# Performance work log

Hardware: AMD Instinct MI355X
Metric: run time of the kernel (lower is better)

Reference implementation:

```python
import jax, jax.numpy as jnp
import numpy as np

B, S, D, FD = 2, 2048, 1024, 4096
EPS_LN = 1e-5


def _l2norm(x):
    n = jnp.linalg.norm(x, axis=-1, keepdims=True)
    return x / jnp.maximum(n, 1e-12)


def _layernorm(x, w, b):
    m = x.mean(-1, keepdims=True)
    v = ((x - m) ** 2).mean(-1, keepdims=True)
    return (x - m) / jnp.sqrt(v + EPS_LN) * w + b


def _spl(x, mu_w, mu_b, gate, proto):
    # cosine-similarity gated linear (SparseProtoLinear)
    scores = _l2norm(x) @ _l2norm(proto).T          # [..., out]
    rw = jax.nn.relu(scores - gate)
    comp = x @ mu_w.T + mu_b
    return comp * rw


def _rotate_half(x):
    h = x.shape[-1] // 2
    return jnp.concatenate([-x[..., h:], x[..., :h]], axis=-1)


def _forward(x, cos, sin,
             ln1_w, ln1_b, ln2_w, ln2_b,
             qkv_mu, qkv_proto, qkv_bias, qkv_gate,
             o_mu, o_proto, o_bias, o_gate,
             f1_mu, f1_proto, f1_bias, f1_gate,
             f2_mu, f2_proto, f2_bias, f2_gate,
             pt_qkv, pt_o, pt_f1, pt_f2,
             pln_qkv_w, pln_qkv_b, pln_o_w, pln_o_b,
             pln_f1_w, pln_f1_b, pln_f2_w, pln_f2_b,
             prev_qkv, prev_o, prev_f1, prev_f2):
    # effective protos: proto_weight + LN(Linear(prev_proto))
    eff_qkv = qkv_proto + _layernorm(prev_qkv @ pt_qkv.T, pln_qkv_w, pln_qkv_b)
    eff_o   = o_proto   + _layernorm(prev_o   @ pt_o.T,   pln_o_w,   pln_o_b)
    eff_f1  = f1_proto  + _layernorm(prev_f1  @ pt_f1.T,  pln_f1_w,  pln_f1_b)
    eff_f2  = f2_proto  + _layernorm(prev_f2  @ pt_f2.T,  pln_f2_w,  pln_f2_b)

    # attention
    attn_in = _layernorm(x, ln1_w, ln1_b)
    m_qkv = _spl(attn_in, qkv_mu, qkv_bias, qkv_gate, eff_qkv)   # [B,S,3D]
    q, k, v = jnp.split(m_qkv, 3, axis=-1)
    c = cos[None]; s = sin[None]
    q = q * c + _rotate_half(q) * s
    k = k * c + _rotate_half(k) * s
    scale = 1.0 / jnp.sqrt(jnp.asarray(D, x.dtype))
    scores = jnp.einsum('bqd,bkd->bqk', q, k) * scale            # [B,S,S]
    causal = jnp.tril(jnp.ones((S, S), dtype=bool))
    scores = jnp.where(causal[None], scores, jnp.finfo(x.dtype).min)
    attn = jax.nn.softmax(scores, axis=-1)
    attn_out = jnp.einsum('bqk,bkd->bqd', attn, v)
    m_o = _spl(attn_out, o_mu, o_bias, o_gate, eff_o)
    x1 = x + m_o

    # ffn (DynamicInfiniteExpert)
    ffn_in = _layernorm(x1, ln2_w, ln2_b)
    m1 = _spl(ffn_in, f1_mu, f1_bias, f1_gate, eff_f1)           # [B,S,FD]
    h = jax.nn.relu(m1)
    m2 = _spl(h, f2_mu, f2_bias, f2_gate, eff_f2)                # [B,S,D]
    return x1 + m2


def setup_inputs() -> dict:
    key = jax.random.key(0)
    ks = iter(jax.random.split(key, 64))

    def nrm(shape, scale=1.0):
        return jax.random.normal(next(ks), shape, dtype=jnp.float32) * scale

    # RoPE tables
    pos = np.arange(S, dtype=np.float32)
    inv_freq = 1.0 / (10000.0 ** (np.arange(0, D, 2, dtype=np.float32) / D))
    freqs = np.outer(pos, inv_freq)
    emb = np.concatenate([freqs, freqs], axis=-1)
    cos = jnp.asarray(np.cos(emb)); sin = jnp.asarray(np.sin(emb))

    sD = 1.0 / np.sqrt(D); sF = 1.0 / np.sqrt(FD)
    inp = {
        'x': nrm((B, S, D)), 'cos': cos, 'sin': sin,
        'ln1_w': jnp.ones((D,)), 'ln1_b': jnp.zeros((D,)),
        'ln2_w': jnp.ones((D,)), 'ln2_b': jnp.zeros((D,)),
        'qkv_mu': nrm((3 * D, D), sD), 'qkv_proto': nrm((3 * D, D), sD),
        'qkv_bias': jnp.zeros((3 * D,)), 'qkv_gate': jnp.zeros((3 * D,)),
        'o_mu': nrm((D, D), sD), 'o_proto': nrm((D, D), sD),
        'o_bias': jnp.zeros((D,)), 'o_gate': jnp.zeros((D,)),
        'f1_mu': nrm((FD, D), sD), 'f1_proto': nrm((FD, D), sD),
        'f1_bias': jnp.zeros((FD,)), 'f1_gate': jnp.zeros((FD,)),
        'f2_mu': nrm((D, FD), sF), 'f2_proto': nrm((D, FD), sF),
        'f2_bias': jnp.zeros((D,)), 'f2_gate': jnp.zeros((D,)),
        'pt_qkv': nrm((D, D), sD), 'pt_o': nrm((D, D), sD),
        'pt_f1': nrm((D, D), sD), 'pt_f2': nrm((FD, FD), sF),
        'pln_qkv_w': jnp.ones((D,)), 'pln_qkv_b': jnp.zeros((D,)),
        'pln_o_w': jnp.ones((D,)), 'pln_o_b': jnp.zeros((D,)),
        'pln_f1_w': jnp.ones((D,)), 'pln_f1_b': jnp.zeros((D,)),
        'pln_f2_w': jnp.ones((FD,)), 'pln_f2_b': jnp.zeros((FD,)),
        'prev_qkv': nrm((3 * D, D), sD), 'prev_o': nrm((D, D), sD),
        'prev_f1': nrm((FD, D), sD), 'prev_f2': nrm((D, FD), sF),
    }
    return inp


def reference(x, cos, sin,
              ln1_w, ln1_b, ln2_w, ln2_b,
              qkv_mu, qkv_proto, qkv_bias, qkv_gate,
              o_mu, o_proto, o_bias, o_gate,
              f1_mu, f1_proto, f1_bias, f1_gate,
              f2_mu, f2_proto, f2_bias, f2_gate,
              pt_qkv, pt_o, pt_f1, pt_f2,
              pln_qkv_w, pln_qkv_b, pln_o_w, pln_o_b,
              pln_f1_w, pln_f1_b, pln_f2_w, pln_f2_b,
              prev_qkv, prev_o, prev_f1, prev_f2):
    return _forward(x, cos, sin, ln1_w, ln1_b, ln2_w, ln2_b,
                    qkv_mu, qkv_proto, qkv_bias, qkv_gate,
                    o_mu, o_proto, o_bias, o_gate,
                    f1_mu, f1_proto, f1_bias, f1_gate,
                    f2_mu, f2_proto, f2_bias, f2_gate,
                    pt_qkv, pt_o, pt_f1, pt_f2,
                    pln_qkv_w, pln_qkv_b, pln_o_w, pln_o_b,
                    pln_f1_w, pln_f1_b, pln_f2_w, pln_f2_b,
                    prev_qkv, prev_o, prev_f1, prev_f2)
```

## Files before the change

kernel.cpp:

```cpp
#include <hip/hip_runtime.h>
#include <cstdint>

typedef unsigned short u16;
typedef __attribute__((ext_vector_type(8))) short sh8;
typedef __attribute__((ext_vector_type(4))) float f32x4;

struct __align__(8) us4 { u16 x, y, z, w; };

__device__ __forceinline__ u16 f2bf(float f) {
  unsigned u = __float_as_uint(f);
  u += 0x7FFFu + ((u >> 16) & 1u);
  return (u16)(u >> 16);
}
__device__ __forceinline__ float bf2f(u16 h) {
  return __uint_as_float((unsigned)h << 16);
}

__device__ __forceinline__ float blk_sum(float v, float* red) {
#pragma unroll
  for (int o = 32; o; o >>= 1) v += __shfl_xor(v, o);
  __syncthreads();
  if ((threadIdx.x & 63) == 0) red[threadIdx.x >> 6] = v;
  __syncthreads();
  return red[0] + red[1] + red[2] + red[3];
}
__device__ __forceinline__ float blk_max(float v, float* red) {
#pragma unroll
  for (int o = 32; o; o >>= 1) v = fmaxf(v, __shfl_xor(v, o));
  __syncthreads();
  if ((threadIdx.x & 63) == 0) red[threadIdx.x >> 6] = v;
  __syncthreads();
  return fmaxf(fmaxf(red[0], red[1]), fmaxf(red[2], red[3]));
}

__global__ void cvt_bf16(const float* __restrict__ S, u16* __restrict__ D, long n4) {
  long i = (long)blockIdx.x * blockDim.x + threadIdx.x;
  if (i >= n4) return;
  float4 v = ((const float4*)S)[i];
  us4 o; o.x = f2bf(v.x); o.y = f2bf(v.y); o.z = f2bf(v.z); o.w = f2bf(v.w);
  ((us4*)D)[i] = o;
}

__global__ void cvt_str(const float* __restrict__ S, u16* __restrict__ Dst,
                        int K, long ostride) {
  int row = blockIdx.x;
  const float* s = S + (size_t)row * K;
  u16* d = Dst + (size_t)row * ostride;
  for (int c = threadIdx.x << 2; c < K; c += 1024) {
    float4 v = *(const float4*)(s + c);
    us4 o; o.x = f2bf(v.x); o.y = f2bf(v.y); o.z = f2bf(v.z); o.w = f2bf(v.w);
    *(us4*)(d + c) = o;
  }
}

__global__ void fillv(float* __restrict__ o, long n, float v) {
  long i = (long)blockIdx.x * blockDim.x + threadIdx.x;
  if (i < n) o[i] = v;
}

#define GL16(gp, lp)                                                        \
  __builtin_amdgcn_global_load_lds(                                         \
      (const __attribute__((address_space(1))) void*)(gp),                  \
      (__attribute__((address_space(3))) void*)(lp), 16, 0, 0)

#define G256_PROLOG()                                                          \
  extern __shared__ u16 lds[];                                                 \
  int tid = threadIdx.x;                                                       \
  int wid = tid >> 6, lane = tid & 63;                                         \
  int wm = wid >> 2, wn = wid & 3;                                             \
  int bm = blockIdx.x, bn = blockIdx.y;                                        \
  int k0s = 0, nt;                                                             \
  if (kchunk) {                                                                \
    k0s = blockIdx.z * kchunk;                                                 \
    nt = kchunk >> 5;                                                          \
  } else {                                                                     \
    nt = K >> 5;                                                               \
  }                                                                            \
  const size_t baseArow = (size_t)bm * 256;                                    \
  const size_t baseBrow = (size_t)bn * 256;                                    \
  int ci = (wid << 6) + lane;                                                  \
  int rowS = ci >> 2;                                                          \
  int kcS = (ci ^ (ci >> 3)) & 3;                                              \
  const u16* gA0 = A + (baseArow + rowS) * lda + k0s + kcS * 8;                \
  const u16* gA1 = gA0 + (size_t)128 * lda;                                    \
  const u16* gB0 = B + (baseBrow + rowS) * ldb + k0s + kcS * 8;                \
  const u16* gB1 = gB0 + (size_t)128 * ldb;                                    \
  u16* dBase = lds + (wid << 9);                                               \
  int l15 = lane & 15, l4 = lane >> 4;                                         \
  int aoff[8], boff[4];                                                        \
  _Pragma("unroll") for (int fr = 0; fr < 8; ++fr) {                           \
    int by = (wm * 128 + fr * 16 + l15) * 64 + l4 * 16;                        \
    aoff[fr] = (by ^ (((by >> 7) & 3) << 4)) >> 1;                             \
  }                                                                            \
  _Pragma("unroll") for (int fc = 0; fc < 4; ++fc) {                           \
    int by = (wn * 64 + fc * 16 + l15) * 64 + l4 * 16;                         \
    boff[fc] = 8192 + ((by ^ (((by >> 7) & 3) << 4)) >> 1);                    \
  }                                                                            \
  f32x4 acc[8][4];                                                             \
  const f32x4 zf = {0.f, 0.f, 0.f, 0.f};                                       \
  _Pragma("unroll") for (int i = 0; i < 8; ++i)                                \
    _Pragma("unroll") for (int j = 0; j < 4; ++j) acc[i][j] = zf;

#define STAGE256(ts)                                                  \
  do {                                                                \
    int ss_ = (ts) & 3;                                               \
    int kk_ = (ts) << 5;                                              \
    u16* d_ = dBase + ss_ * 16384;                                    \
    GL16(gA0 + kk_, d_);                                              \
    GL16(gA1 + kk_, d_ + 4096);                                       \
    GL16(gB0 + kk_, d_ + 8192);                                       \
    GL16(gB1 + kk_, d_ + 12288);                                      \
  } while (0)

#define G256_KLOOP()                                                           \
  STAGE256(0);                                                                 \
  STAGE256(1);                                                                 \
  STAGE256(2);                                                                 \
  asm volatile("s_waitcnt vmcnt(8)" ::: "memory");                             \
  __builtin_amdgcn_s_barrier();                                                \
  __builtin_amdgcn_sched_barrier(0);                                           \
  for (int t = 0; t < nt; ++t) {                                               \
    int ts = t + 3;                                                            \
    if (ts < nt) STAGE256(ts);                                                 \
    const u16* sl = lds + (t & 3) * 16384;                                     \
    sh8 af[8], bfv[4];                                                         \
    _Pragma("unroll") for (int fc = 0; fc < 4; ++fc)                           \
        bfv[fc] = *(const sh8*)(sl + boff[fc]);                                \
    _Pragma("unroll") for (int fr = 0; fr < 8; ++fr)                           \
        af[fr] = *(const sh8*)(sl + aoff[fr]);                                 \
    __builtin_amdgcn_s_setprio(1);                                             \
    _Pragma("unroll") for (int fr = 0; fr < 8; ++fr)                           \
      _Pragma("unroll") for (int fc = 0; fc < 4; ++fc)                         \
        acc[fr][fc] = __builtin_amdgcn_mfma_f32_16x16x32_bf16(                 \
            af[fr], bfv[fc], acc[fr][fc], 0, 0, 0);                            \
    __builtin_amdgcn_s_setprio(0);                                             \
    int rem = nt - 2 - t;                                                      \
    if (rem >= 2)      asm volatile("s_waitcnt vmcnt(8)" ::: "memory");        \
    else if (rem == 1) asm volatile("s_waitcnt vmcnt(4)" ::: "memory");        \
    else if (rem == 0) asm volatile("s_waitcnt vmcnt(0)" ::: "memory");        \
    if (t < nt - 1) {                                                          \
      __builtin_amdgcn_s_barrier();                                            \
      __builtin_amdgcn_sched_barrier(0);                                       \
    }                                                                          \
  }

template <typename CT>
__global__ __launch_bounds__(512, 1) void gemm256(
    const u16* __restrict__ A, const u16* __restrict__ B, CT* __restrict__ C,
    int M, int N, int K, int lda, int ldb, int kchunk) {
  if (kchunk) C += (size_t)blockIdx.z * M * (size_t)N;
  G256_PROLOG();
  G256_KLOOP();
  int cr = l4 << 2, cc = l15;
  const size_t rbase = baseArow + wm * 128 + cr;
  const size_t cbase = baseBrow + wn * 64 + cc;
#pragma unroll
  for (int fr = 0; fr < 8; ++fr)
#pragma unroll
    for (int fc = 0; fc < 4; ++fc) {
      size_t cb = (rbase + fr * 16) * (size_t)N + cbase + fc * 16;
#pragma unroll
      for (int r = 0; r < 4; ++r) {
        float v = acc[fr][fc][r];
        if constexpr (sizeof(CT) == 2) C[cb + (size_t)r * N] = (CT)f2bf(v);
        else                           C[cb + (size_t)r * N] = v;
      }
    }
}

__global__ __launch_bounds__(512, 1) void gemm256_spl(
    const u16* __restrict__ A, const u16* __restrict__ B, u16* __restrict__ out,
    int M, int N, int K, int lda, int ldb, int kchunk,
    const float* __restrict__ bias, const float* __restrict__ gate,
    const float* __restrict__ rn, const float* __restrict__ cn, int relu_out) {
  G256_PROLOG();
  G256_KLOOP();
  int cr = l4 << 2, cc = l15;
  const size_t rbase = baseArow + wm * 128 + cr;
  const size_t cbase = baseBrow + wn * 64 + cc;
  const int F = N >> 1;
  bool evenL = (cc & 1) == 0;
  float bb[4], gg[4], nn[4];
  int ft[4];
#pragma unroll
  for (int fc = 0; fc < 4; ++fc) {
    ft[fc] = (int)((cbase + fc * 16) >> 1);
    bb[fc] = bias[ft[fc]]; gg[fc] = gate[ft[fc]]; nn[fc] = cn[ft[fc]];
  }
#pragma unroll
  for (int fr = 0; fr < 8; ++fr)
#pragma unroll
    for (int r = 0; r < 4; ++r) {
      size_t row = rbase + fr * 16 + r;
      float rr = rn[row];
#pragma unroll
      for (int fc = 0; fc < 4; ++fc) {
        float mine = acc[fr][fc][r];
        float other = __shfl_xor(mine, 1);
        float comp = evenL ? mine : other;
        float dots = evenL ? other : mine;
        float sc = dots / (rr * nn[fc]);
        float v = (comp + bb[fc]) * fmaxf(sc - gg[fc], 0.f);
        if (relu_out) v = fmaxf(v, 0.f);
        if (evenL) out[row * (size_t)F + ft[fc]] = f2bf(v);
      }
    }
}

template <typename CT>
__global__ __launch_bounds__(256, 2) void gemm_bt(
    const u16* __restrict__ A, const u16* __restrict__ B, CT* __restrict__ C,
    int M, int N, int K, int lda, int ldb,
    int mode, long zsA, long zsB, long zsC) {
  int bm, bn;
  int z = blockIdx.z;
  if (mode == 3) {
    int t = blockIdx.x;
    int m = (int)floorf((sqrtf(8.f * t + 1.f) - 1.f) * 0.5f);
    while ((m + 1) * (m + 2) / 2 <= t) ++m;
    while (m * (m + 1) / 2 > t) --m;
    bm = m; bn = t - m * (m + 1) / 2;
  } else {
    bm = blockIdx.x; bn = blockIdx.y;
  }
  int k0s = 0, k0e = K;
  if (mode == 1) {
    int kc = K / gridDim.z;
    k0s = z * kc; k0e = k0s + kc;
    C += (size_t)z * M * (size_t)N;
  } else if (mode == 2 || mode == 3) {
    A += (size_t)z * zsA; B += (size_t)z * zsB; C += (size_t)z * zsC;
  } else if (mode == 4) {
    A += (size_t)z * zsA; B += (size_t)z * zsB; C += (size_t)z * zsC;
    k0e = (bm + 1) * 128;
  } else if (mode == 5) {
    int Mz = (int)((zsB >> (z * 16)) & 0xFFFF);
    if (bm * 128 >= Mz) return;
    A += (size_t)z * zsA; B += (size_t)z * 1048576; C += (size_t)z * zsC;
  }

  __shared__ __align__(16) u16 As[128 * 32];
  __shared__ __align__(16) u16 Bs[128 * 32];
  int tid = threadIdx.x, wid = tid >> 6, lane = tid & 63;
  int wr = (wid >> 1) << 6, wc = (wid & 1) << 6;
  int lr = lane & 15, lk = (lane >> 4) << 3;

  f32x4 acc[4][4];
  const f32x4 zf = {0.f, 0.f, 0.f, 0.f};
#pragma unroll
  for (int i = 0; i < 4; ++i)
#pragma unroll
    for (int j = 0; j < 4; ++j) acc[i][j] = zf;

  int r0 = tid >> 2, c0 = (tid & 3) << 3;
  const size_t baseA = (size_t)bm * 128, baseB = (size_t)bn * 128;
  const u16* Ab = A + baseA * lda;
  const u16* Bp = B + baseB * ldb;

  for (int k0 = k0s; k0 < k0e; k0 += 32) {
    GL16(Ab + (size_t)r0 * lda + k0 + c0, As + (wid << 9));
    GL16(Ab + (size_t)(64 + r0) * lda + k0 + c0, As + 2048 + (wid << 9));
    GL16(Bp + (size_t)r0 * ldb + k0 + c0, Bs + (wid << 9));
    GL16(Bp + (size_t)(64 + r0) * ldb + k0 + c0, Bs + 2048 + (wid << 9));
    __syncthreads();
    sh8 af[4], bfr[4];
#pragma unroll
    for (int f = 0; f < 4; ++f) {
      af[f]  = *(const sh8*)(As + (wr + f * 16 + lr) * 32 + lk);
      bfr[f] = *(const sh8*)(Bs + (wc + f * 16 + lr) * 32 + lk);
    }
#pragma unroll
    for (int i = 0; i < 4; ++i)
#pragma unroll
      for (int j = 0; j < 4; ++j)
        acc[i][j] = __builtin_amdgcn_mfma_f32_16x16x32_bf16(af[i], bfr[j], acc[i][j], 0, 0, 0);
    __syncthreads();
  }

  int cr = (lane >> 4) << 2, cc = lane & 15;
#pragma unroll
  for (int i = 0; i < 4; ++i)
#pragma unroll
    for (int j = 0; j < 4; ++j) {
      size_t cb = (baseA + wr + i * 16 + cr) * (size_t)N + (baseB + wc + j * 16 + cc);
#pragma unroll
      for (int r = 0; r < 4; ++r) {
        float v = acc[i][j][r];
        if constexpr (sizeof(CT) == 2) C[cb + (size_t)r * N] = (CT)f2bf(v);
        else                           C[cb + (size_t)r * N] = v;
      }
    }
}

__global__ void ln_rows(const float* __restrict__ X, const float* __restrict__ w,
                        const float* __restrict__ b, u16* __restrict__ Y,
                        float* __restrict__ norms, int C) {
  __shared__ float red[4];
  int row = blockIdx.x;
  const float* x = X + (size_t)row * C;
  int nv = C >> 2;
  float s = 0.f, ss = 0.f;
  for (int i = threadIdx.x; i < nv; i += 256) {
    float4 v = ((const float4*)x)[i];
    s += v.x + v.y + v.z + v.w;
    ss += v.x * v.x + v.y * v.y + v.z * v.z + v.w * v.w;
  }
  s = blk_sum(s, red);
  ss = blk_sum(ss, red);
  float mean = s / C;
  float inv = rsqrtf(fmaxf(ss / C - mean * mean, 0.f) + 1e-5f);
  float nrm = 0.f;
  for (int i = threadIdx.x; i < nv; i += 256) {
    float4 v = ((const float4*)x)[i];
    float4 wv = ((const float4*)w)[i];
    float4 bv = ((const float4*)b)[i];
    float y0 = (v.x - mean) * inv * wv.x + bv.x;
    float y1 = (v.y - mean) * inv * wv.y + bv.y;
    float y2 = (v.z - mean) * inv * wv.z + bv.z;
    float y3 = (v.w - mean) * inv * wv.w + bv.w;
    nrm += y0 * y0 + y1 * y1 + y2 * y2 + y3 * y3;
    us4 o; o.x = f2bf(y0); o.y = f2bf(y1); o.z = f2bf(y2); o.w = f2bf(y3);
    ((us4*)(Y + (size_t)row * C))[i] = o;
  }
  nrm = blk_sum(nrm, red);
  if (threadIdx.x == 0) norms[row] = fmaxf(sqrtf(nrm), 1e-12f);
}

__global__ void ln_add_norm(const u16* __restrict__ T0, const u16* __restrict__ T1,
                            const float* __restrict__ P,
                            const float* __restrict__ w, const float* __restrict__ b,
                            u16* __restrict__ E, float* __restrict__ norms, int C,
                            long ostride) {
  __shared__ float red[4];
  int row = blockIdx.x;
  const us4* t0 = (const us4*)(T0 + (size_t)row * C);
  const us4* t1 = T1 ? (const us4*)(T1 + (size_t)row * C) : nullptr;
  const float* p = P + (size_t)row * C;
  int nv = C >> 2;
  float s = 0.f, ss = 0.f;
  for (int i = threadIdx.x; i < nv; i += 256) {
    us4 v = t0[i];
    float f0 = bf2f(v.x), f1 = bf2f(v.y), f2 = bf2f(v.z), f3 = bf2f(v.w);
    if (t1) {
      us4 v1 = t1[i];
      f0 += bf2f(v1.x); f1 += bf2f(v1.y); f2 += bf2f(v1.z); f3 += bf2f(v1.w);
    }
    s += f0 + f1 + f2 + f3;
    ss += f0 * f0 + f1 * f1 + f2 * f2 + f3 * f3;
  }
  s = blk_sum(s, red);
  ss = blk_sum(ss, red);
  float mean = s / C;
  float inv = rsqrtf(fmaxf(ss / C - mean * mean, 0.f) + 1e-5f);
  float nrm = 0.f;
  for (int i = threadIdx.x; i < nv; i += 256) {
    us4 v = t0[i];
    float f0 = bf2f(v.x), f1 = bf2f(v.y), f2 = bf2f(v.z), f3 = bf2f(v.w);
    if (t1) {
      us4 v1 = t1[i];
      f0 += bf2f(v1.x); f1 += bf2f(v1.y); f2 += bf2f(v1.z); f3 += bf2f(v1.w);
    }
    float4 pv = ((const float4*)p)[i];
    float4 wv = ((const float4*)w)[i];
    float4 bv = ((const float4*)b)[i];
    float y0 = pv.x + (f0 - mean) * inv * wv.x + bv.x;
    float y1 = pv.y + (f1 - mean) * inv * wv.y + bv.y;
    float y2 = pv.z + (f2 - mean) * inv * wv.z + bv.z;
    float y3 = pv.w + (f3 - mean) * inv * wv.w + bv.w;
    nrm += y0 * y0 + y1 * y1 + y2 * y2 + y3 * y3;
    us4 o; o.x = f2bf(y0); o.y = f2bf(y1); o.z = f2bf(y2); o.w = f2bf(y3);
    *(us4*)(E + (size_t)row * ostride + (i << 2)) = o;
  }
  nrm = blk_sum(nrm, red);
  if (threadIdx.x == 0) norms[row] = fmaxf(sqrtf(nrm), 1e-12f);
}

__global__ void rownorm_bf(const u16* __restrict__ X, float* __restrict__ norms, int C) {
  __shared__ float red[4];
  int row = blockIdx.x;
  const us4* x = (const us4*)(X + (size_t)row * C);
  int nv = C >> 2;
  float nrm = 0.f;
  for (int i = threadIdx.x; i < nv; i += 256) {
    us4 v = x[i];
    float a = bf2f(v.x), b = bf2f(v.y), c = bf2f(v.z), d = bf2f(v.w);
    nrm += a * a + b * b + c * c + d * d;
  }
  nrm = blk_sum(nrm, red);
  if (threadIdx.x == 0) norms[row] = fmaxf(sqrtf(nrm), 1e-12f);
}

__device__ __forceinline__ void epi4(const u16* gr, int C, int c, float rr,
                                     const float* bias, const float* gate,
                                     const float* cn, float* o) {
  us4 cv = *(const us4*)(gr + c);
  us4 dv = *(const us4*)(gr + C + c);
  float4 bv = *(const float4*)(bias + c);
  float4 gv = *(const float4*)(gate + c);
  float4 nv = *(const float4*)(cn + c);
  float cf[4] = {bf2f(cv.x), bf2f(cv.y), bf2f(cv.z), bf2f(cv.w)};
  float df[4] = {bf2f(dv.x), bf2f(dv.y), bf2f(dv.z), bf2f(dv.w)};
  float bb[4] = {bv.x, bv.y, bv.z, bv.w};
  float gg[4] = {gv.x, gv.y, gv.z, gv.w};
  float nn[4] = {nv.x, nv.y, nv.z, nv.w};
#pragma unroll
  for (int j = 0; j < 4; ++j) {
    float sc = df[j] / (rr * nn[j]);
    o[j] = (cf[j] + bb[j]) * fmaxf(sc - gg[j], 0.f);
  }
}

__global__ void rope_ip(u16* __restrict__ MQ, const float* __restrict__ CT_,
                        const float* __restrict__ ST_) {
  long t = (long)blockIdx.x * blockDim.x + threadIdx.x;
  int i = (int)(t & 511);
  long row = t >> 9;
  int s = (int)(row & 2047);
  u16* base = MQ + row * 3072;
  float c0 = CT_[(size_t)s * 1024 + i], c1 = CT_[(size_t)s * 1024 + 512 + i];
  float s0 = ST_[(size_t)s * 1024 + i], s1 = ST_[(size_t)s * 1024 + 512 + i];
  float q0 = bf2f(base[i]), q1 = bf2f(base[512 + i]);
  base[i]        = f2bf(q0 * c0 - q1 * s0);
  base[512 + i]  = f2bf(q1 * c1 + q0 * s1);
  float k0 = bf2f(base[1024 + i]), k1 = bf2f(base[1536 + i]);
  base[1024 + i] = f2bf(k0 * c0 - k1 * s0);
  base[1536 + i] = f2bf(k1 * c1 + k0 * s1);
}

__global__ void spl_o_ln_row(const u16* __restrict__ G, const float* __restrict__ bias,
                             const float* __restrict__ gate, const float* __restrict__ rn,
                             const float* __restrict__ cn, const float* __restrict__ xres,
                             const float* __restrict__ lw, const float* __restrict__ lb,
                             float* __restrict__ X1, u16* __restrict__ Y,
                             float* __restrict__ rn_ffn) {
  __shared__ float red[4];
  int r = blockIdx.x;
  int c = threadIdx.x << 2;
  const u16* gr = G + (size_t)r * 2048;
  float o[4];
  epi4(gr, 1024, c, rn[r], bias, gate, cn, o);
  float4 rv = *(const float4*)(xres + (size_t)r * 1024 + c);
  o[0] += rv.x; o[1] += rv.y; o[2] += rv.z; o[3] += rv.w;
  float4 xo = {o[0], o[1], o[2], o[3]};
  *(float4*)(X1 + (size_t)r * 1024 + c) = xo;
  float s = o[0] + o[1] + o[2] + o[3];
  float ss = o[0] * o[0] + o[1] * o[1] + o[2] * o[2] + o[3] * o[3];
  s = blk_sum(s, red);
  ss = blk_sum(ss, red);
  float mean = s * (1.f / 1024.f);
  float inv = rsqrtf(fmaxf(ss * (1.f / 1024.f) - mean * mean, 0.f) + 1e-5f);
  float4 wv = *(const float4*)(lw + c);
  float4 bv = *(const float4*)(lb + c);
  float ww[4] = {wv.x, wv.y, wv.z, wv.w}, bb[4] = {bv.x, bv.y, bv.z, bv.w};
  float nrm = 0.f;
  us4 ov;
  u16* op = (u16*)&ov;
#pragma unroll
  for (int j = 0; j < 4; ++j) {
    float y = (o[j] - mean) * inv * ww[j] + bb[j];
    nrm += y * y;
    op[j] = f2bf(y);
  }
  *(us4*)(Y + (size_t)r * 1024 + c) = ov;
  nrm = blk_sum(nrm, red);
  if (threadIdx.x == 0) rn_ffn[r] = fmaxf(sqrtf(nrm), 1e-12f);
}

__global__ void spl_epi_p(const u16* __restrict__ G0, const u16* __restrict__ G1,
                          const float* __restrict__ bias, const float* __restrict__ gate,
                          const float* __restrict__ rn, const float* __restrict__ cn,
                          const float* __restrict__ resid, float* __restrict__ out) {
  int r = blockIdx.x;
  int c = threadIdx.x << 2;
  size_t rowb = (size_t)r * 2048;
  us4 c0 = *(const us4*)(G0 + rowb + c);
  us4 c1 = *(const us4*)(G1 + rowb + c);
  us4 d0 = *(const us4*)(G0 + rowb + 1024 + c);
  us4 d1 = *(const us4*)(G1 + rowb + 1024 + c);
  float4 bv = *(const float4*)(bias + c);
  float4 gv = *(const float4*)(gate + c);
  float4 nv = *(const float4*)(cn + c);
  float4 rv = *(const float4*)(resid + (size_t)r * 1024 + c);
  float rr = rn[r];
  float cf[4] = {bf2f(c0.x) + bf2f(c1.x), bf2f(c0.y) + bf2f(c1.y),
                 bf2f(c0.z) + bf2f(c1.z), bf2f(c0.w) + bf2f(c1.w)};
  float df[4] = {bf2f(d0.x) + bf2f(d1.x), bf2f(d0.y) + bf2f(d1.y),
                 bf2f(d0.z) + bf2f(d1.z), bf2f(d0.w) + bf2f(d1.w)};
  float bb[4] = {bv.x, bv.y, bv.z, bv.w};
  float gg[4] = {gv.x, gv.y, gv.z, gv.w};
  float nn[4] = {nv.x, nv.y, nv.z, nv.w};
  float re[4] = {rv.x, rv.y, rv.z, rv.w};
  float4 ov;
  float* op = (float*)&ov;
#pragma unroll
  for (int j = 0; j < 4; ++j) {
    float sc = df[j] / (rr * nn[j]);
    op[j] = (cf[j] + bb[j]) * fmaxf(sc - gg[j], 0.f) + re[j];
  }
  *(float4*)(out + (size_t)r * 1024 + c) = ov;
}

__global__ void vtrans(const u16* __restrict__ MQ, u16* __restrict__ VT) {
  __shared__ u16 tile[32][33];
  int b = blockIdx.z;
  int s0 = blockIdx.x << 5, d0 = blockIdx.y << 5;
  int tx = threadIdx.x, ty = threadIdx.y;
  for (int r = ty; r < 32; r += 8)
    tile[r][tx] = MQ[((size_t)(b * 2048 + s0 + r)) * 3072 + 2048 + d0 + tx];
  __syncthreads();
  for (int r = ty; r < 32; r += 8)
    VT[(size_t)b * 1024 * 2048 + (size_t)(d0 + r) * 2048 + s0 + tx] = tile[tx][r];
}

__global__ void softmax_causal(const float* __restrict__ S, u16* __restrict__ P) {
  __shared__ float red[4];
  int b = blockIdx.x >> 11;
  int q = blockIdx.x & 2047;
  const float* row = S + ((size_t)b << 22) + (size_t)q * 2048;
  u16* prow = P + ((size_t)b << 22) + (size_t)q * 2048;
  int nv = q + 1;
  int wcap = ((q >> 7) + 1) << 7;
  int base = threadIdx.x * 8;
  float e[8];
  float m = -3.4e38f;
  float xv[8];
  bool live = base < nv;
  if (live) {
    float4 a = *(const float4*)(row + base);
    float4 bq = *(const float4*)(row + base + 4);
    xv[0] = a.x; xv[1] = a.y; xv[2] = a.z; xv[3] = a.w;
    xv[4] = bq.x; xv[5] = bq.y; xv[6] = bq.z; xv[7] = bq.w;
#pragma unroll
    for (int j = 0; j < 8; ++j) {
      xv[j] *= 0.03125f;
      if (base + j < nv) m = fmaxf(m, xv[j]);
    }
  }
  m = blk_max(m, red);
  float ssum = 0.f;
#pragma unroll
  for (int j = 0; j < 8; ++j) {
    e[j] = (live && base + j < nv) ? __expf(xv[j] - m) : 0.f;
    ssum += e[j];
  }
  ssum = blk_sum(ssum, red);
  float invs = 1.f / ssum;
  if (base < wcap) {
    us4 o;
    o.x = f2bf(e[0] * invs); o.y = f2bf(e[1] * invs);
    o.z = f2bf(e[2] * invs); o.w = f2bf(e[3] * invs);
    ((us4*)prow)[threadIdx.x * 2] = o;
    o.x = f2bf(e[4] * invs); o.y = f2bf(e[5] * invs);
    o.z = f2bf(e[6] * invs); o.w = f2bf(e[7] * invs);
    ((us4*)prow)[threadIdx.x * 2 + 1] = o;
  }
}

extern "C" void kernel_launch(void* const* d_in, const int* in_sizes, int n_in,
                              void* d_out, int out_size, void* d_ws, size_t ws_size,
                              hipStream_t stream) {
  (void)in_sizes;
  const float* x         = (const float*)d_in[0];
  const float* cosT      = (const float*)d_in[1];
  const float* sinT      = (const float*)d_in[2];
  const float* ln1_w     = (const float*)d_in[3];
  const float* ln1_b     = (const float*)d_in[4];
  const float* ln2_w     = (const float*)d_in[5];
  const float* ln2_b     = (const float*)d_in[6];
  const float* qkv_mu    = (const float*)d_in[7];
  const float* qkv_proto = (const float*)d_in[8];
  const float* qkv_bias  = (const float*)d_in[9];
  const float* qkv_gate  = (const float*)d_in[10];
  const float* o_mu      = (const float*)d_in[11];
  const float* o_proto   = (const float*)d_in[12];
  const float* o_bias    = (const float*)d_in[13];
  const float* o_gate    = (const float*)d_in[14];
  const float* f1_mu     = (const float*)d_in[15];
  const float* f1_proto  = (const float*)d_in[16];
  const float* f1_bias   = (const float*)d_in[17];
  const float* f1_gate   = (const float*)d_in[18];
  const float* f2_mu     = (const float*)d_in[19];
  const float* f2_proto  = (const float*)d_in[20];
  const float* f2_bias   = (const float*)d_in[21];
  const float* f2_gate   = (const float*)d_in[22];
  const float* pt_qkv    = (const float*)d_in[23];
  const float* pt_o      = (const float*)d_in[24];
  const float* pt_f1     = (const float*)d_in[25];
  const float* pt_f2     = (const float*)d_in[26];
  const float* pln_qkv_w = (const float*)d_in[27];
  const float* pln_qkv_b = (const float*)d_in[28];
  const float* pln_o_w   = (const float*)d_in[29];
  const float* pln_o_b   = (const float*)d_in[30];
  const float* pln_f1_w  = (const float*)d_in[31];
  const float* pln_f1_b  = (const float*)d_in[32];
  const float* pln_f2_w  = (const float*)d_in[33];
  const float* pln_f2_b  = (const float*)d_in[34];
  const float* prev_qkv  = (const float*)d_in[35];
  const float* prev_o    = (const float*)d_in[36];
  const float* prev_f1   = (const float*)d_in[37];
  const float* prev_f2   = (const float*)d_in[38];

  const long D = 1024, TD = 3072, FD = 4096, R = 4096;

  char* W = (char*)d_ws;
  size_t off = 0;
  auto alloc = [&](size_t bytes) {
    void* p = W + off;
    off = (off + bytes + 255) & ~(size_t)255;
    return p;
  };
  char* GOUT = (char*)alloc(67108864);
  u16*  RC   = (u16*)alloc(33554432);
  u16*  wq   = (u16*)alloc(2 * TD * D * 2);
  u16*  wo   = (u16*)alloc(2 * D * D * 2);
  u16*  wf1  = (u16*)alloc(2 * FD * D * 2);
  u16*  wf2  = (u16*)alloc(2 * D * FD * 2);
  float* X1  = (float*)alloc(R * D * 4);
  u16*  P1   = (u16*)alloc(R * D * 2);
  u16*  VT   = (u16*)alloc(2 * D * 2048 * 2);
  u16*  AOB  = (u16*)alloc(R * D * 2);
  float* pnq     = (float*)alloc(TD * 4);
  float* pno     = (float*)alloc(D * 4);
  float* pnf1    = (float*)alloc(FD * 4);
  float* pnf2    = (float*)alloc(D * 4);
  float* rn_ain  = (float*)alloc(R * 4);
  float* rn_aout = (float*)alloc(R * 4);
  float* rn_ffn  = (float*)alloc(R * 4);
  float* rn_h    = (float*)alloc(R * 4);
  size_t need = off;

  if (n_in < 39 || need > ws_size) {
    long n = out_size;
    fillv<<<dim3((unsigned)((n + 255) / 256)), 256, 0, stream>>>((float*)d_out, n, 12345.0f);
    return;
  }

  u16* SA = (u16*)GOUT;
  u16* SB = (u16*)(GOUT + 25165824);
  float* SCORES = (float*)GOUT;
  u16* PB = (u16*)(GOUT + 33554432);

  auto cvt = [&](const float* s, u16* d, long n) {
    long n4 = n >> 2;
    cvt_bf16<<<dim3((unsigned)((n4 + 255) / 256)), 256, 0, stream>>>(s, d, n4);
  };

  cvt(prev_f1,  SA,            FD * D);
  cvt(prev_qkv, SA + 4194304,  TD * D);
  cvt(prev_o,   SA + 8388608,  D * D);
  cvt(pt_f1,    SB,            D * D);
  cvt(pt_qkv,   SB + 1048576,  D * D);
  cvt(pt_o,     SB + 2097152,  D * D);
  {
    long Mz = 4096L | (3072L << 16) | (1024L << 32);
    gemm_bt<u16><<<dim3(32, 8, 3), 256, 0, stream>>>(
        SA, SB, RC, 4096, 1024, 1024, 1024, 1024, 5, 4194304, Mz, 4194304);
  }
  ln_add_norm<<<4096, 256, 0, stream>>>(RC, nullptr, f1_proto, pln_f1_w, pln_f1_b,
                                        wf1 + 1024, pnf1, 1024, 2048);
  ln_add_norm<<<3072, 256, 0, stream>>>(RC + 4194304, nullptr, qkv_proto, pln_qkv_w,
                                        pln_qkv_b, wq + 1024, pnq, 1024, 2048);
  ln_add_norm<<<1024, 256, 0, stream>>>(RC + 8388608, nullptr, o_proto, pln_o_w,
                                        pln_o_b, wo + (size_t)D * D, pno, 1024, 1024);
  cvt(prev_f2, SA, D * FD);
  cvt(pt_f2,   SB, (long)FD * FD);
  gemm_bt<u16><<<dim3(8, 32, 2), 256, 0, stream>>>(
      SA, SB, RC, 1024, 4096, 4096, 4096, 4096, 1, 0, 0, 0);
  ln_add_norm<<<1024, 256, 0, stream>>>(RC, RC + 4194304, f2_proto, pln_f2_w, pln_f2_b,
                                        wf2 + (size_t)D * FD, pnf2, 4096, 4096);
  cvt_str<<<3072, 256, 0, stream>>>(qkv_mu, wq, 1024, 2048);
  cvt_str<<<4096, 256, 0, stream>>>(f1_mu, wf1, 1024, 2048);
  cvt(o_mu,   wo, D * D);
  cvt(f2_mu,  wf2, D * FD);

  ln_rows<<<4096, 256, 0, stream>>>(x, ln1_w, ln1_b, P1, rn_ain, 1024);
  gemm256_spl<<<dim3(16, 24), 512, 131072, stream>>>(
      P1, wq, RC, 4096, 6144, 1024, 1024, 1024, 0,
      qkv_bias, qkv_gate, rn_ain, pnq, 0);
  rope_ip<<<dim3((unsigned)((R * 512) / 256)), 256, 0, stream>>>(RC, cosT, sinT);

  vtrans<<<dim3(64, 32, 2), dim3(32, 8), 0, stream>>>(RC, VT);
  gemm_bt<float><<<dim3(136, 1, 2), 256, 0, stream>>>(
      RC, RC + 1024, SCORES, 2048, 2048, 1024, 3072, 3072,
      3, 2048L * 3072, 2048L * 3072, 1L << 22);
  softmax_causal<<<4096, 256, 0, stream>>>(SCORES, PB);
  gemm_bt<u16><<<dim3(16, 8, 2), 256, 0, stream>>>(
      PB, VT, AOB, 2048, 1024, 2048, 2048, 2048,
      4, 1L << 22, 1024L * 2048, 2048L * 1024);
  rownorm_bf<<<4096, 256, 0, stream>>>(AOB, rn_aout, 1024);

  gemm_bt<u16><<<dim3(32, 16, 1), 256, 0, stream>>>(
      AOB, wo, (u16*)GOUT, 4096, 2048, 1024, 1024, 1024, 0, 0, 0, 0);
  spl_o_ln_row<<<4096, 256, 0, stream>>>(
      (u16*)GOUT, o_bias, o_gate, rn_aout, pno, x, ln2_w, ln2_b, X1, P1, rn_ffn);

  gemm256_spl<<<dim3(16, 32), 512, 131072, stream>>>(
      P1, wf1, RC, 4096, 8192, 1024, 1024, 1024, 0,
      f1_bias, f1_gate, rn_ffn, pnf1, 1);
  rownorm_bf<<<4096, 256, 0, stream>>>(RC, rn_h, 4096);
  gemm256<u16><<<dim3(16, 8, 2), 512, 131072, stream>>>(
      RC, wf2, (u16*)GOUT, 4096, 2048, 4096, 4096, 4096, 2048);
  spl_epi_p<<<4096, 256, 0, stream>>>(
      (u16*)GOUT, (u16*)GOUT + 8388608, f2_bias, f2_gate, rn_h, pnf2,
      X1, (float*)d_out);
}
```

Baseline: 636.4 us.

## Split SPL epilogues out of GEMMs, batch conversions, store inverse norms

```diff
diff --git a/kernel.cpp b/kernel.cpp
--- a/kernel.cpp
+++ b/kernel.cpp
@@ -14,6 +14,9 @@
 }
 __device__ __forceinline__ float bf2f(u16 h) {
   return __uint_as_float((unsigned)h << 16);
+}
+__device__ __forceinline__ float invnorm(float nrm) {
+  return fminf(rsqrtf(nrm), 1e12f);
 }
 
 __device__ __forceinline__ float blk_sum(float v, float* red) {
@@ -33,29 +36,23 @@
   return fmaxf(fmaxf(red[0], red[1]), fmaxf(red[2], red[3]));
 }
 
-__global__ void cvt_bf16(const float* __restrict__ S, u16* __restrict__ D, long n4) {
-  long i = (long)blockIdx.x * blockDim.x + threadIdx.x;
-  if (i >= n4) return;
-  float4 v = ((const float4*)S)[i];
-  us4 o; o.x = f2bf(v.x); o.y = f2bf(v.y); o.z = f2bf(v.z); o.w = f2bf(v.w);
-  ((us4*)D)[i] = o;
-}
-
-__global__ void cvt_str(const float* __restrict__ S, u16* __restrict__ Dst,
-                        int K, long ostride) {
-  int row = blockIdx.x;
-  const float* s = S + (size_t)row * K;
-  u16* d = Dst + (size_t)row * ostride;
-  for (int c = threadIdx.x << 2; c < K; c += 1024) {
-    float4 v = *(const float4*)(s + c);
-    us4 o; o.x = f2bf(v.x); o.y = f2bf(v.y); o.z = f2bf(v.z); o.w = f2bf(v.w);
-    *(us4*)(d + c) = o;
-  }
-}
-
 __global__ void fillv(float* __restrict__ o, long n, float v) {
   long i = (long)blockIdx.x * blockDim.x + threadIdx.x;
   if (i < n) o[i] = v;
+}
+
+struct CvtN10 {
+  const float* s[10];
+  u16* d[10];
+  long n4[10];
+};
+__global__ void cvt_many(CvtN10 c) {
+  int z = blockIdx.y;
+  long i = (long)blockIdx.x * blockDim.x + threadIdx.x;
+  if (i >= c.n4[z]) return;
+  float4 v = ((const float4*)c.s[z])[i];
+  us4 o; o.x = f2bf(v.x); o.y = f2bf(v.y); o.z = f2bf(v.z); o.w = f2bf(v.w);
+  ((us4*)c.d[z])[i] = o;
 }
 
 #define GL16(gp, lp)                                                        \
@@ -168,45 +165,6 @@
     }
 }
 
-__global__ __launch_bounds__(512, 1) void gemm256_spl(
-    const u16* __restrict__ A, const u16* __restrict__ B, u16* __restrict__ out,
-    int M, int N, int K, int lda, int ldb, int kchunk,
-    const float* __restrict__ bias, const float* __restrict__ gate,
-    const float* __restrict__ rn, const float* __restrict__ cn, int relu_out) {
-  G256_PROLOG();
-  G256_KLOOP();
-  int cr = l4 << 2, cc = l15;
-  const size_t rbase = baseArow + wm * 128 + cr;
-  const size_t cbase = baseBrow + wn * 64 + cc;
-  const int F = N >> 1;
-  bool evenL = (cc & 1) == 0;
-  float bb[4], gg[4], nn[4];
-  int ft[4];
-#pragma unroll
-  for (int fc = 0; fc < 4; ++fc) {
-    ft[fc] = (int)((cbase + fc * 16) >> 1);
-    bb[fc] = bias[ft[fc]]; gg[fc] = gate[ft[fc]]; nn[fc] = cn[ft[fc]];
-  }
-#pragma unroll
-  for (int fr = 0; fr < 8; ++fr)
-#pragma unroll
-    for (int r = 0; r < 4; ++r) {
-      size_t row = rbase + fr * 16 + r;
-      float rr = rn[row];
-#pragma unroll
-      for (int fc = 0; fc < 4; ++fc) {
-        float mine = acc[fr][fc][r];
-        float other = __shfl_xor(mine, 1);
-        float comp = evenL ? mine : other;
-        float dots = evenL ? other : mine;
-        float sc = dots / (rr * nn[fc]);
-        float v = (comp + bb[fc]) * fmaxf(sc - gg[fc], 0.f);
-        if (relu_out) v = fmaxf(v, 0.f);
-        if (evenL) out[row * (size_t)F + ft[fc]] = f2bf(v);
-      }
-    }
-}
-
 template <typename CT>
 __global__ __launch_bounds__(256, 2) void gemm_bt(
     const u16* __restrict__ A, const u16* __restrict__ B, CT* __restrict__ C,
@@ -323,14 +281,13 @@
     ((us4*)(Y + (size_t)row * C))[i] = o;
   }
   nrm = blk_sum(nrm, red);
-  if (threadIdx.x == 0) norms[row] = fmaxf(sqrtf(nrm), 1e-12f);
+  if (threadIdx.x == 0) norms[row] = invnorm(nrm);
 }
 
 __global__ void ln_add_norm(const u16* __restrict__ T0, const u16* __restrict__ T1,
                             const float* __restrict__ P,
                             const float* __restrict__ w, const float* __restrict__ b,
-                            u16* __restrict__ E, float* __restrict__ norms, int C,
-                            long ostride) {
+                            u16* __restrict__ E, float* __restrict__ norms, int C) {
   __shared__ float red[4];
   int row = blockIdx.x;
   const us4* t0 = (const us4*)(T0 + (size_t)row * C);
@@ -369,10 +326,40 @@
     float y3 = pv.w + (f3 - mean) * inv * wv.w + bv.w;
     nrm += y0 * y0 + y1 * y1 + y2 * y2 + y3 * y3;
     us4 o; o.x = f2bf(y0); o.y = f2bf(y1); o.z = f2bf(y2); o.w = f2bf(y3);
-    *(us4*)(E + (size_t)row * ostride + (i << 2)) = o;
+    *(us4*)(E + (size_t)row * C + (i << 2)) = o;
   }
   nrm = blk_sum(nrm, red);
-  if (threadIdx.x == 0) norms[row] = fmaxf(sqrtf(nrm), 1e-12f);
+  if (threadIdx.x == 0) norms[row] = invnorm(nrm);
+}
+
+struct Lan3 {
+  const u16* T[3];
+  const float* P[3]; const float* w[3]; const float* b[3];
+  u16* E[3]; float* nr[3]; int M[3];
+};
+__global__ void lan_many(Lan3 L) {
+  __shared__ float red[4];
+  int z = blockIdx.y;
+  int row = blockIdx.x;
+  if (row >= L.M[z]) return;
+  int i = threadIdx.x;
+  us4 v = ((const us4*)(L.T[z] + (size_t)row * 1024))[i];
+  float f0 = bf2f(v.x), f1 = bf2f(v.y), f2 = bf2f(v.z), f3 = bf2f(v.w);
+  float s = blk_sum(f0 + f1 + f2 + f3, red);
+  float ss = blk_sum(f0 * f0 + f1 * f1 + f2 * f2 + f3 * f3, red);
+  float mean = s * (1.f / 1024.f);
+  float inv = rsqrtf(fmaxf(ss * (1.f / 1024.f) - mean * mean, 0.f) + 1e-5f);
+  float4 pv = ((const float4*)(L.P[z] + (size_t)row * 1024))[i];
+  float4 wv = ((const float4*)L.w[z])[i];
+  float4 bv = ((const float4*)L.b[z])[i];
+  float y0 = pv.x + (f0 - mean) * inv * wv.x + bv.x;
+  float y1 = pv.y + (f1 - mean) * inv * wv.y + bv.y;
+  float y2 = pv.z + (f2 - mean) * inv * wv.z + bv.z;
+  float y3 = pv.w + (f3 - mean) * inv * wv.w + bv.w;
+  us4 o; o.x = f2bf(y0); o.y = f2bf(y1); o.z = f2bf(y2); o.w = f2bf(y3);
+  ((us4*)(L.E[z] + (size_t)row * 1024))[i] = o;
+  float nrm = blk_sum(y0 * y0 + y1 * y1 + y2 * y2 + y3 * y3, red);
+  if (threadIdx.x == 0) L.nr[z][row] = invnorm(nrm);
 }
 
 __global__ void rownorm_bf(const u16* __restrict__ X, float* __restrict__ norms, int C) {
@@ -387,7 +374,7 @@
     nrm += a * a + b * b + c * c + d * d;
   }
   nrm = blk_sum(nrm, red);
-  if (threadIdx.x == 0) norms[row] = fmaxf(sqrtf(nrm), 1e-12f);
+  if (threadIdx.x == 0) norms[row] = invnorm(nrm);
 }
 
 __device__ __forceinline__ void epi4(const u16* gr, int C, int c, float rr,
@@ -405,26 +392,78 @@
   float nn[4] = {nv.x, nv.y, nv.z, nv.w};
 #pragma unroll
   for (int j = 0; j < 4; ++j) {
-    float sc = df[j] / (rr * nn[j]);
+    float sc = df[j] * (rr * nn[j]);
     o[j] = (cf[j] + bb[j]) * fmaxf(sc - gg[j], 0.f);
   }
 }
 
-__global__ void rope_ip(u16* __restrict__ MQ, const float* __restrict__ CT_,
-                        const float* __restrict__ ST_) {
-  long t = (long)blockIdx.x * blockDim.x + threadIdx.x;
-  int i = (int)(t & 511);
-  long row = t >> 9;
-  int s = (int)(row & 2047);
-  u16* base = MQ + row * 3072;
-  float c0 = CT_[(size_t)s * 1024 + i], c1 = CT_[(size_t)s * 1024 + 512 + i];
-  float s0 = ST_[(size_t)s * 1024 + i], s1 = ST_[(size_t)s * 1024 + 512 + i];
-  float q0 = bf2f(base[i]), q1 = bf2f(base[512 + i]);
-  base[i]        = f2bf(q0 * c0 - q1 * s0);
-  base[512 + i]  = f2bf(q1 * c1 + q0 * s1);
-  float k0 = bf2f(base[1024 + i]), k1 = bf2f(base[1536 + i]);
-  base[1024 + i] = f2bf(k0 * c0 - k1 * s0);
-  base[1536 + i] = f2bf(k1 * c1 + k0 * s1);
+__global__ void spl_rope_row(const u16* __restrict__ G, const float* __restrict__ bias,
+                             const float* __restrict__ gate, const float* __restrict__ rn,
+                             const float* __restrict__ cn, const float* __restrict__ CT_,
+                             const float* __restrict__ ST_, u16* __restrict__ MQ) {
+  int r = blockIdx.x;
+  int s = r & 2047;
+  const u16* gr = G + (size_t)r * 6144;
+  u16* outr = MQ + (size_t)r * 3072;
+  float rr = rn[r];
+  int t = threadIdx.x;
+
+  int qk = (t >> 7);
+  int c = qk * 1024 + ((t & 127) << 2);
+  int d = c - qk * 1024;
+  float a0[4], a1[4];
+  epi4(gr, 3072, c, rr, bias, gate, cn, a0);
+  epi4(gr, 3072, c + 512, rr, bias, gate, cn, a1);
+  const float* ct = CT_ + (size_t)s * 1024;
+  const float* st = ST_ + (size_t)s * 1024;
+  float4 c0 = *(const float4*)(ct + d);
+  float4 s0 = *(const float4*)(st + d);
+  float4 c1 = *(const float4*)(ct + d + 512);
+  float4 s1 = *(const float4*)(st + d + 512);
+  float cc0[4] = {c0.x, c0.y, c0.z, c0.w}, ss0[4] = {s0.x, s0.y, s0.z, s0.w};
+  float cc1[4] = {c1.x, c1.y, c1.z, c1.w}, ss1[4] = {s1.x, s1.y, s1.z, s1.w};
+  us4 o0, o1;
+  o0.x = f2bf(a0[0] * cc0[0] - a1[0] * ss0[0]);
+  o0.y = f2bf(a0[1] * cc0[1] - a1[1] * ss0[1]);
+  o0.z = f2bf(a0[2] * cc0[2] - a1[2] * ss0[2]);
+  o0.w = f2bf(a0[3] * cc0[3] - a1[3] * ss0[3]);
+  o1.x = f2bf(a1[0] * cc1[0] + a0[0] * ss1[0]);
+  o1.y = f2bf(a1[1] * cc1[1] + a0[1] * ss1[1]);
+  o1.z = f2bf(a1[2] * cc1[2] + a0[2] * ss1[2]);
+  o1.w = f2bf(a1[3] * cc1[3] + a0[3] * ss1[3]);
+  *(us4*)(outr + c) = o0;
+  *(us4*)(outr + c + 512) = o1;
+
+  int cv_ = 2048 + (t << 2);
+  float vv[4];
+  epi4(gr, 3072, cv_, rr, bias, gate, cn, vv);
+  us4 ov; ov.x = f2bf(vv[0]); ov.y = f2bf(vv[1]); ov.z = f2bf(vv[2]); ov.w = f2bf(vv[3]);
+  *(us4*)(outr + cv_) = ov;
+}
+
+__global__ void spl_f1_row(const u16* __restrict__ G, const float* __restrict__ bias,
+                           const float* __restrict__ gate, const float* __restrict__ rn,
+                           const float* __restrict__ cn, u16* __restrict__ H,
+                           float* __restrict__ rn_h) {
+  __shared__ float red[4];
+  int r = blockIdx.x;
+  const u16* gr = G + (size_t)r * 8192;
+  u16* hr = H + (size_t)r * 4096;
+  float rr = rn[r];
+  float nrm = 0.f;
+  for (int c = threadIdx.x << 2; c < 4096; c += 1024) {
+    float o[4];
+    epi4(gr, 4096, c, rr, bias, gate, cn, o);
+#pragma unroll
+    for (int j = 0; j < 4; ++j) {
+      o[j] = fmaxf(o[j], 0.f);
+      nrm += o[j] * o[j];
+    }
+    us4 ov; ov.x = f2bf(o[0]); ov.y = f2bf(o[1]); ov.z = f2bf(o[2]); ov.w = f2bf(o[3]);
+    *(us4*)(hr + c) = ov;
+  }
+  nrm = blk_sum(nrm, red);
+  if (threadIdx.x == 0) rn_h[r] = invnorm(nrm);
 }
 
 __global__ void spl_o_ln_row(const u16* __restrict__ G, const float* __restrict__ bias,
@@ -463,7 +502,7 @@
   }
   *(us4*)(Y + (size_t)r * 1024 + c) = ov;
   nrm = blk_sum(nrm, red);
-  if (threadIdx.x == 0) rn_ffn[r] = fmaxf(sqrtf(nrm), 1e-12f);
+  if (threadIdx.x == 0) rn_ffn[r] = invnorm(nrm);
 }
 
 __global__ void spl_epi_p(const u16* __restrict__ G0, const u16* __restrict__ G1,
@@ -494,7 +533,7 @@
   float* op = (float*)&ov;
 #pragma unroll
   for (int j = 0; j < 4; ++j) {
-    float sc = df[j] / (rr * nn[j]);
+    float sc = df[j] * (rr * nn[j]);
     op[j] = (cf[j] + bb[j]) * fmaxf(sc - gg[j], 0.f) + re[j];
   }
   *(float4*)(out + (size_t)r * 1024 + c) = ov;
@@ -640,44 +679,51 @@
   float* SCORES = (float*)GOUT;
   u16* PB = (u16*)(GOUT + 33554432);
 
-  auto cvt = [&](const float* s, u16* d, long n) {
-    long n4 = n >> 2;
-    cvt_bf16<<<dim3((unsigned)((n4 + 255) / 256)), 256, 0, stream>>>(s, d, n4);
-  };
-
-  cvt(prev_f1,  SA,            FD * D);
-  cvt(prev_qkv, SA + 4194304,  TD * D);
-  cvt(prev_o,   SA + 8388608,  D * D);
-  cvt(pt_f1,    SB,            D * D);
-  cvt(pt_qkv,   SB + 1048576,  D * D);
-  cvt(pt_o,     SB + 2097152,  D * D);
+  {
+    CvtN10 c;
+    c.s[0] = prev_f1;  c.d[0] = SA;            c.n4[0] = (FD * D) >> 2;
+    c.s[1] = prev_qkv; c.d[1] = SA + 4194304;  c.n4[1] = (TD * D) >> 2;
+    c.s[2] = prev_o;   c.d[2] = SA + 8388608;  c.n4[2] = (D * D) >> 2;
+    c.s[3] = pt_f1;    c.d[3] = SB;            c.n4[3] = (D * D) >> 2;
+    c.s[4] = pt_qkv;   c.d[4] = SB + 1048576;  c.n4[4] = (D * D) >> 2;
+    c.s[5] = pt_o;     c.d[5] = SB + 2097152;  c.n4[5] = (D * D) >> 2;
+    c.s[6] = qkv_mu;   c.d[6] = wq;            c.n4[6] = (TD * D) >> 2;
+    c.s[7] = f1_mu;    c.d[7] = wf1;           c.n4[7] = (FD * D) >> 2;
+    c.s[8] = o_mu;     c.d[8] = wo;            c.n4[8] = (D * D) >> 2;
+    c.s[9] = f2_mu;    c.d[9] = wf2;           c.n4[9] = (D * FD) >> 2;
+    cvt_many<<<dim3(4096, 10), 256, 0, stream>>>(c);
+  }
   {
     long Mz = 4096L | (3072L << 16) | (1024L << 32);
     gemm_bt<u16><<<dim3(32, 8, 3), 256, 0, stream>>>(
         SA, SB, RC, 4096, 1024, 1024, 1024, 1024, 5, 4194304, Mz, 4194304);
   }
-  ln_add_norm<<<4096, 256, 0, stream>>>(RC, nullptr, f1_proto, pln_f1_w, pln_f1_b,
-                                        wf1 + 1024, pnf1, 1024, 2048);
-  ln_add_norm<<<3072, 256, 0, stream>>>(RC + 4194304, nullptr, qkv_proto, pln_qkv_w,
-                                        pln_qkv_b, wq + 1024, pnq, 1024, 2048);
-  ln_add_norm<<<1024, 256, 0, stream>>>(RC + 8388608, nullptr, o_proto, pln_o_w,
-                                        pln_o_b, wo + (size_t)D * D, pno, 1024, 1024);
-  cvt(prev_f2, SA, D * FD);
-  cvt(pt_f2,   SB, (long)FD * FD);
+  {
+    Lan3 L;
+    L.T[0] = RC;           L.P[0] = f1_proto;  L.w[0] = pln_f1_w;  L.b[0] = pln_f1_b;
+    L.E[0] = wf1 + (size_t)FD * D;  L.nr[0] = pnf1;  L.M[0] = 4096;
+    L.T[1] = RC + 4194304; L.P[1] = qkv_proto; L.w[1] = pln_qkv_w; L.b[1] = pln_qkv_b;
+    L.E[1] = wq + (size_t)TD * D;   L.nr[1] = pnq;   L.M[1] = 3072;
+    L.T[2] = RC + 8388608; L.P[2] = o_proto;   L.w[2] = pln_o_w;   L.b[2] = pln_o_b;
+    L.E[2] = wo + (size_t)D * D;    L.nr[2] = pno;   L.M[2] = 1024;
+    lan_many<<<dim3(4096, 3), 256, 0, stream>>>(L);
+  }
+  {
+    CvtN10 c = {};
+    c.s[0] = prev_f2; c.d[0] = SA; c.n4[0] = (D * FD) >> 2;
+    c.s[1] = pt_f2;   c.d[1] = SB; c.n4[1] = ((long)FD * FD) >> 2;
+    cvt_many<<<dim3(16384, 2), 256, 0, stream>>>(c);
+  }
   gemm_bt<u16><<<dim3(8, 32, 2), 256, 0, stream>>>(
       SA, SB, RC, 1024, 4096, 4096, 4096, 4096, 1, 0, 0, 0);
   ln_add_norm<<<1024, 256, 0, stream>>>(RC, RC + 4194304, f2_proto, pln_f2_w, pln_f2_b,
-                                        wf2 + (size_t)D * FD, pnf2, 4096, 4096);
-  cvt_str<<<3072, 256, 0, stream>>>(qkv_mu, wq, 1024, 2048);
-  cvt_str<<<4096, 256, 0, stream>>>(f1_mu, wf1, 1024, 2048);
-  cvt(o_mu,   wo, D * D);
-  cvt(f2_mu,  wf2, D * FD);
+                                        wf2 + (size_t)D * FD, pnf2, 4096);
 
   ln_rows<<<4096, 256, 0, stream>>>(x, ln1_w, ln1_b, P1, rn_ain, 1024);
-  gemm256_spl<<<dim3(16, 24), 512, 131072, stream>>>(
-      P1, wq, RC, 4096, 6144, 1024, 1024, 1024, 0,
-      qkv_bias, qkv_gate, rn_ain, pnq, 0);
-  rope_ip<<<dim3((unsigned)((R * 512) / 256)), 256, 0, stream>>>(RC, cosT, sinT);
+  gemm256<u16><<<dim3(16, 24), 512, 131072, stream>>>(
+      P1, wq, (u16*)GOUT, 4096, 6144, 1024, 1024, 1024, 0);
+  spl_rope_row<<<4096, 256, 0, stream>>>(
+      (u16*)GOUT, qkv_bias, qkv_gate, rn_ain, pnq, cosT, sinT, RC);
 
   vtrans<<<dim3(64, 32, 2), dim3(32, 8), 0, stream>>>(RC, VT);
   gemm_bt<float><<<dim3(136, 1, 2), 256, 0, stream>>>(
@@ -694,10 +740,10 @@
   spl_o_ln_row<<<4096, 256, 0, stream>>>(
       (u16*)GOUT, o_bias, o_gate, rn_aout, pno, x, ln2_w, ln2_b, X1, P1, rn_ffn);
 
-  gemm256_spl<<<dim3(16, 32), 512, 131072, stream>>>(
-      P1, wf1, RC, 4096, 8192, 1024, 1024, 1024, 0,
-      f1_bias, f1_gate, rn_ffn, pnf1, 1);
-  rownorm_bf<<<4096, 256, 0, stream>>>(RC, rn_h, 4096);
+  gemm256<u16><<<dim3(16, 32), 512, 131072, stream>>>(
+      P1, wf1, (u16*)GOUT, 4096, 8192, 1024, 1024, 1024, 0);
+  spl_f1_row<<<4096, 256, 0, stream>>>(
+      (u16*)GOUT, f1_bias, f1_gate, rn_ffn, pnf1, RC, rn_h);
   gemm256<u16><<<dim3(16, 8, 2), 512, 131072, stream>>>(
       RC, wf2, (u16*)GOUT, 4096, 2048, 4096, 4096, 4096, 2048);
   spl_epi_p<<<4096, 256, 0, stream>>>(
```

Result: faster. 558.3 us (-12.3%).
